# Kernel optimization log

Measured on AMD Instinct MI355X. Metric: run time of the kernel, lower is better.

## Reference

```python
import jax, jax.numpy as jnp
import numpy as np

EPS = 1e-5

def _ln(x, g, b):
    mu = x.mean(-1, keepdims=True)
    var = ((x - mu) ** 2).mean(-1, keepdims=True)
    return (x - mu) * jax.lax.rsqrt(var + EPS) * g + b

def setup_inputs() -> dict:
    B, K, D, H, T = 64, 64, 128, 128, 4
    key = jax.random.key(0)
    ks = jax.random.split(key, 20)
    s = 0.02
    inp = {
        "slots": jax.random.normal(ks[0], (B, K, D), jnp.float32),
        "edge_probs": jax.random.uniform(ks[1], (B, K, K), jnp.float32),
        "edge_types": jax.random.uniform(ks[2], (B, K, K, T), jnp.float32),
        # f_self: LayerNorm(D) -> Linear(D,H) -> ReLU -> Linear(H,D)
        "ls_g": jnp.ones((D,), jnp.float32),
        "ls_b": jnp.zeros((D,), jnp.float32),
        "ws1": jax.random.normal(ks[3], (D, H), jnp.float32) * s,
        "bs1": jnp.zeros((H,), jnp.float32),
        "ws2": jax.random.normal(ks[4], (H, D), jnp.float32) * s,
        "bs2": jnp.zeros((D,), jnp.float32),
        # f_inter[tau]: Linear(2D,H) -> ReLU -> Linear(H,H) -> ReLU -> Linear(H,D), stacked over T
        "wi1": jax.random.normal(ks[5], (T, 2 * D, H), jnp.float32) * s,
        "bi1": jnp.zeros((T, H), jnp.float32),
        "wi2": jax.random.normal(ks[6], (T, H, H), jnp.float32) * s,
        "bi2": jnp.zeros((T, H), jnp.float32),
        "wi3": jax.random.normal(ks[7], (T, H, D), jnp.float32) * s,
        "bi3": jnp.zeros((T, D), jnp.float32),
        # update_mlp: LayerNorm(2D) -> Linear(2D,H) -> ReLU -> Linear(H,D)
        "lu_g": jnp.ones((2 * D,), jnp.float32),
        "lu_b": jnp.zeros((2 * D,), jnp.float32),
        "wu1": jax.random.normal(ks[8], (2 * D, H), jnp.float32) * s,
        "bu1": jnp.zeros((H,), jnp.float32),
        "wu2": jax.random.normal(ks[9], (H, D), jnp.float32) * s,
        "bu2": jnp.zeros((D,), jnp.float32),
    }
    return inp

NUM_MP = 2

def reference(slots, edge_probs, edge_types, ls_g, ls_b, ws1, bs1, ws2, bs2,
              wi1, bi1, wi2, bi2, wi3, bi3, lu_g, lu_b, wu1, bu1, wu2, bu2):
    B, K, D = slots.shape
    T = edge_types.shape[-1]
    h = slots
    for _ in range(NUM_MP):
        # f_self
        delta_self = jax.nn.relu(_ln(h, ls_g, ls_b) @ ws1 + bs1) @ ws2 + bs2
        # all-pairs features: cat[b,i,j] = [h[b,i] (sender), h[b,j] (receiver)]
        sender = jnp.broadcast_to(h[:, :, None, :], (B, K, K, D))
        receiver = jnp.broadcast_to(h[:, None, :, :], (B, K, K, D))
        pair = jnp.concatenate([sender, receiver], axis=-1)  # [B,K,K,2D]
        delta_inter = jnp.zeros_like(h)
        for tau in range(T):
            x = jax.nn.relu(pair @ wi1[tau] + bi1[tau])
            x = jax.nn.relu(x @ wi2[tau] + bi2[tau])
            eff = x @ wi3[tau] + bi3[tau]  # [B,K,K,D]
            w = edge_probs[..., None] * edge_types[..., tau, None]  # [B,K,K,1]
            delta_inter = delta_inter + (eff * w).sum(axis=1)  # sum over sender i
        combined = jnp.concatenate([h + delta_self, delta_inter], axis=-1)
        update = jax.nn.relu(_ln(combined, lu_g, lu_b) @ wu1 + bu1) @ wu2 + bu2
        h = h + update  # residual=True
    return h
```

## Files before the change

### kernel.cpp

```cpp
#include <hip/hip_runtime.h>
#include <hip/hip_fp16.h>

#define BATCH 64
#define KSLOT 64
#define DDIM  128
#define HDIM  128
#define TTYPE 4
#define NSLOT (BATCH*KSLOT)
#define EPSLN 1e-5f
#define YROW  544

typedef _Float16 v8h __attribute__((ext_vector_type(8)));
typedef _Float16 v4h __attribute__((ext_vector_type(4)));
typedef _Float16 v2h __attribute__((ext_vector_type(2)));
typedef float    v4f __attribute__((ext_vector_type(4)));

__device__ __forceinline__ float waveAllSum(float v) {
    #pragma unroll
    for (int m = 1; m < 64; m <<= 1) v += __shfl_xor(v, m, 64);
    return v;
}

__global__ __launch_bounds__(256) void k_wconv(
        const float* __restrict__ ws1, const float* __restrict__ wi1,
        const float* __restrict__ ws2, const float* __restrict__ wu1,
        const float* __restrict__ wu2, const float* __restrict__ wi3,
        const float* __restrict__ wi2, const float* __restrict__ bi1,
        const float* __restrict__ bi3,
        const float* __restrict__ ep, const float* __restrict__ et,
        __half* __restrict__ ws1T, __half* __restrict__ wi1catT,
        __half* __restrict__ ws2T, __half* __restrict__ wu1T,
        __half* __restrict__ wu2T, __half* __restrict__ w3catT,
        __half* __restrict__ w2T16, float* __restrict__ biascat,
        __half* __restrict__ wPre) {
    __shared__ __align__(16) float tile[128*132];
    int bx = blockIdx.x, tid = threadIdx.x;
    if (bx >= 22) {
        int bx2 = bx - 22, b = bx2 >> 2, chunk = bx2 & 3;
        const float4* etb = (const float4*)(et + (size_t)b*16384);
        const float*  epb = ep + (size_t)b*4096;
        __half* w0 = wPre + ((size_t)0*BATCH + b)*4096;
        __half* w1 = wPre + ((size_t)1*BATCH + b)*4096;
        __half* w2 = wPre + ((size_t)2*BATCH + b)*4096;
        __half* w3 = wPre + ((size_t)3*BATCH + b)*4096;
        int c0 = chunk*1024;
        for (int c = c0 + tid; c < c0 + 1024; c += 256) {
            float wv = epb[c];
            float4 e = etb[c];
            w0[c] = __float2half(wv * e.x);
            w1[c] = __float2half(wv * e.y);
            w2[c] = __float2half(wv * e.z);
            w3[c] = __float2half(wv * e.w);
        }
        return;
    }
    if (bx == 21) {
        for (int idx = tid; idx < 128*32; idx += 256) {
            int o = idx >> 5, c = idx & 31;
            w3catT[(size_t)o*YROW + 512 + c] = (c < 4) ? __float2half(bi3[c*DDIM + o]) : __float2half(0.f);
        }
        for (int idx = tid; idx < 1024; idx += 256) {
            int th = idx >> 7, o = idx & 127;
            biascat[idx] = (th & 1) ? bi1[(th>>1)*HDIM + o] : 0.f;
        }
        return;
    }
    const float* src; __half* dst; int dstride = 128, dcol = 0;
    if (bx == 0)      { src = ws1; dst = ws1T; }
    else if (bx <= 8) { int th = bx-1, tau = th>>1, half = th&1;
                        src = wi1 + ((size_t)tau*256 + half*128)*128;
                        dst = wi1catT + (size_t)th*128*128; }
    else if (bx == 9) { src = ws2; dst = ws2T; }
    else if (bx ==10) { src = wu2; dst = wu2T; }
    else if (bx <=12) { int hh = bx-11; src = wu1 + (size_t)hh*128*128;
                        dst = wu1T; dstride = 256; dcol = hh*128; }
    else if (bx <=16) { int tau = bx-13; src = wi3 + (size_t)tau*16384;
                        dst = w3catT; dstride = YROW; dcol = tau*128; }
    else              { int tau = bx-17; src = wi2 + (size_t)tau*16384;
                        dst = w2T16 + (size_t)tau*16384; }
    for (int idx = tid; idx < 4096; idx += 256) {
        int r = idx >> 5, c4 = idx & 31;
        *(float4*)&tile[r*132 + c4*4] = *(const float4*)&src[(size_t)r*128 + c4*4];
    }
    __syncthreads();
    for (int idx = tid; idx < 8192; idx += 256) {
        int n = idx >> 6, kp = idx & 63;
        __half2 p = __floats2half2_rn(tile[(2*kp)*132 + n], tile[(2*kp+1)*132 + n]);
        *(__half2*)&dst[(size_t)n*dstride + dcol + 2*kp] = p;
    }
}

#define LROW 136

__device__ __forceinline__ void cluster4(v4f& p0, v4f& p1, v4f& p2, v4f& p3,
                                         const v8h x[4], const v8h bf[4][4],
                                         const v4f bias[4]) {
    p0 = bias[0]; p1 = bias[1]; p2 = bias[2]; p3 = bias[3];
    #pragma unroll
    for (int ks = 0; ks < 4; ks++) {
        p0 = __builtin_amdgcn_mfma_f32_16x16x32_f16(x[ks], bf[0][ks], p0, 0, 0, 0);
        p1 = __builtin_amdgcn_mfma_f32_16x16x32_f16(x[ks], bf[1][ks], p1, 0, 0, 0);
        p2 = __builtin_amdgcn_mfma_f32_16x16x32_f16(x[ks], bf[2][ks], p2, 0, 0, 0);
        p3 = __builtin_amdgcn_mfma_f32_16x16x32_f16(x[ks], bf[3][ks], p3, 0, 0, 0);
    }
}

__device__ __forceinline__ void epi4(v4h yacch[4], v4h& wsacch,
                                     const v4f& p0, const v4f& p1,
                                     const v4f& p2, const v4f& p3, v4h wv) {
    const v4h zero4h = {0,0,0,0};
    #define EPI1(P, OT) { \
        v2h lo = __builtin_bit_cast(v2h, __builtin_amdgcn_cvt_pkrtz(P[0], P[1])); \
        v2h hi = __builtin_bit_cast(v2h, __builtin_amdgcn_cvt_pkrtz(P[2], P[3])); \
        v4h rel = {lo[0], lo[1], hi[0], hi[1]}; \
        rel = __builtin_elementwise_max(rel, zero4h); \
        yacch[OT] = yacch[OT] + wv * rel; }
    EPI1(p0, 0) EPI1(p1, 1) EPI1(p2, 2) EPI1(p3, 3)
    #undef EPI1
    wsacch = wsacch + wv;
}

__global__ __launch_bounds__(512) void k_pair(
        const float* __restrict__ h,
        const __half* __restrict__ wi1catT,
        const float* __restrict__ biascat,
        const __half* __restrict__ w2T16,
        const float* __restrict__ bi2,
        const __half* __restrict__ wPre,
        __half* __restrict__ Ycat) {
    __shared__ __align__(16) _Float16 w2T[HDIM*LROW];
    __shared__ __align__(16) _Float16 Cs[KSLOT*LROW];
    __shared__ __align__(16) _Float16 As[KSLOT*LROW];
    __shared__ __align__(16) _Float16 wS[KSLOT*KSLOT];
    __shared__ __align__(16) _Float16 hs[KSLOT*136];
    int bx = blockIdx.x, b = bx >> 2, tau = bx & 3;
    int tid = threadIdx.x, lane = tid & 63, w = tid >> 6;
    int jt = w >> 1, oh = w & 1, quad = lane >> 4, n = lane & 15;

    for (int idx = tid; idx < 2048; idx += 512) {
        int o = idx >> 4, seg = (idx & 15)*8;
        *(v8h*)&w2T[o*LROW + seg] = *(const v8h*)&w2T16[((size_t)tau*128 + o)*128 + seg];
    }
    {
        int row = tid >> 3, c0 = (tid & 7)*16;
        const float* hp = &h[(size_t)(b*KSLOT + row)*128 + c0];
        #pragma unroll
        for (int q = 0; q < 4; q++) {
            float4 f = *(const float4*)&hp[q*4];
            *(__half2*)&hs[row*136 + c0 + q*4]     = __floats2half2_rn(f.x, f.y);
            *(__half2*)&hs[row*136 + c0 + q*4 + 2] = __floats2half2_rn(f.z, f.w);
        }
    }
    {
        int base = tid*8;
        *(v8h*)&wS[base] = *(const v8h*)&wPre[((size_t)tau*BATCH + b)*4096 + base];
    }
    __syncthreads();

    {
        int hf = w >> 2, rt = w & 3;
        const __half* wb = wi1catT + (size_t)(tau*2 + hf)*128*128;
        const float* bcp = biascat + (tau*2 + hf)*128;
        _Float16* dst = hf ? Cs : As;
        v8h afr[4];
        #pragma unroll
        for (int ks = 0; ks < 4; ks++)
            afr[ks] = *(const v8h*)&hs[(rt*16 + n)*136 + ks*32 + quad*8];
        #pragma unroll
        for (int ot = 0; ot < 8; ot++) {
            float b0 = bcp[ot*16 + n];
            v4f acc = (v4f){b0, b0, b0, b0};
            #pragma unroll
            for (int ks = 0; ks < 4; ks++)
                acc = __builtin_amdgcn_mfma_f32_16x16x32_f16(
                    afr[ks], *(const v8h*)&wb[(size_t)(ot*16 + n)*128 + ks*32 + quad*8], acc, 0, 0, 0);
            #pragma unroll
            for (int r = 0; r < 4; r++)
                dst[(rt*16 + quad*4 + r)*LROW + ot*16 + n] = (_Float16)acc[r];
        }
    }
    __syncthreads();

    v8h bfrag[4][4];
    #pragma unroll
    for (int ot = 0; ot < 4; ot++)
        #pragma unroll
        for (int ks = 0; ks < 4; ks++)
            bfrag[ot][ks] = *(const v8h*)&w2T[(oh*64 + ot*16 + n)*LROW + ks*32 + quad*8];
    v8h cfrag[4];
    #pragma unroll
    for (int ks = 0; ks < 4; ks++)
        cfrag[ks] = *(const v8h*)&Cs[(jt*16 + n)*LROW + ks*32 + quad*8];
    v4f biasvec[4];
    #pragma unroll
    for (int ot = 0; ot < 4; ot++) {
        float b0 = bi2[tau*HDIM + oh*64 + ot*16 + n];
        biasvec[ot] = (v4f){b0, b0, b0, b0};
    }

    v4h yacch[4];
    #pragma unroll
    for (int ot = 0; ot < 4; ot++) yacch[ot] = (v4h){0,0,0,0};
    v4h wsacch = (v4h){0,0,0,0};
    const v8h zero8 = {0,0,0,0,0,0,0,0};

    #define LOADA(DST, WV, I) { int _i = (I); \
        DST[0] = *(const v8h*)&As[_i*LROW +  0 + quad*8]; \
        DST[1] = *(const v8h*)&As[_i*LROW + 32 + quad*8]; \
        DST[2] = *(const v8h*)&As[_i*LROW + 64 + quad*8]; \
        DST[3] = *(const v8h*)&As[_i*LROW + 96 + quad*8]; \
        WV = *(const v4h*)&wS[_i*KSLOT + jt*16 + quad*4]; }

    v8h aA[4], aB[4], xA[4], xB[4];
    v4h wvA, wvB, wvEA, wvEB;
    LOADA(aA, wvA, 0)
    LOADA(aB, wvB, 1)
    #pragma unroll
    for (int ks = 0; ks < 4; ks++)
        xA[ks] = __builtin_elementwise_max(aA[ks] + cfrag[ks], zero8);
    v4f pA0, pA1, pA2, pA3, pB0, pB1, pB2, pB3;

    for (int ii = 0; ii < 32; ++ii) {
        int i = ii*2;
        wvEA = wvA;
        { int i2 = (i+2 < 64) ? (i+2) : 63; LOADA(aA, wvA, i2) }
        cluster4(pA0, pA1, pA2, pA3, xA, bfrag, biasvec);
        #pragma unroll
        for (int ks = 0; ks < 4; ks++)
            xB[ks] = __builtin_elementwise_max(aB[ks] + cfrag[ks], zero8);
        epi4(yacch, wsacch, pA0, pA1, pA2, pA3, wvEA);
        wvEB = wvB;
        { int i3 = (i+3 < 64) ? (i+3) : 63; LOADA(aB, wvB, i3) }
        cluster4(pB0, pB1, pB2, pB3, xB, bfrag, biasvec);
        #pragma unroll
        for (int ks = 0; ks < 4; ks++)
            xA[ks] = __builtin_elementwise_max(aA[ks] + cfrag[ks], zero8);
        epi4(yacch, wsacch, pB0, pB1, pB2, pB3, wvEB);
    }
    #undef LOADA

    #pragma unroll
    for (int r = 0; r < 4; r++) {
        int j = jt*16 + quad*4 + r;
        __half* yb = Ycat + (size_t)(b*KSLOT + j)*YROW + tau*128 + oh*64;
        #pragma unroll
        for (int ot = 0; ot < 4; ot++)
            yb[ot*16 + n] = __float2half((float)yacch[ot][r]);
    }
    if (oh == 0 && n == 0) {
        #pragma unroll
        for (int r = 0; r < 4; r++)
            Ycat[(size_t)(b*KSLOT + jt*16 + quad*4 + r)*YROW + 512 + tau] = __float2half((float)wsacch[r]);
    }
    if (tau == 0 && oh == 1 && n == 0) {
        const v4h z4 = {0,0,0,0};
        #pragma unroll
        for (int r = 0; r < 4; r++) {
            _Float16* pz = (_Float16*)(Ycat + (size_t)(b*KSLOT + jt*16 + quad*4 + r)*YROW + 516);
            #pragma unroll
            for (int c = 0; c < 28; c += 4) *(v4h*)&pz[c] = z4;
        }
    }
}

__global__ __launch_bounds__(512, 2) void k_mega(
        const __half* __restrict__ Ycat, const __half* __restrict__ w3catT,
        const float* __restrict__ ls_g, const float* __restrict__ ls_b,
        const __half* __restrict__ ws1T, const float* __restrict__ bs1,
        const __half* __restrict__ ws2T, const float* __restrict__ bs2,
        const float* __restrict__ g, const float* __restrict__ bb,
        const __half* __restrict__ wu1T, const float* __restrict__ bu1,
        const __half* __restrict__ wu2T, const float* __restrict__ bu2,
        const float* __restrict__ h, float* __restrict__ hout) {
    __shared__ __align__(16) _Float16 Ys[16*552];
    __shared__ __align__(16) float    Crow[16*260];
    __shared__ __align__(16) float    Hrow[16*132];
    __shared__ __align__(16) _Float16 Xs[16*136];
    __shared__ __align__(16) _Float16 Ts[16*136];
    __shared__ __align__(16) _Float16 Xa[16*264];
    __shared__ __align__(16) _Float16 Ut[16*136];
    int tid = threadIdx.x, lane = tid & 63, w = tid >> 6;
    int n = lane & 15, quad = lane >> 4;
    int row0 = blockIdx.x*16;

    for (int u = tid; u < 1024; u += 512) {
        int r = u >> 6, seg = (u & 63)*8;
        *(v8h*)&Ys[r*552 + seg] = *(const v8h*)&Ycat[(size_t)(row0 + r)*YROW + seg];
    }
    if (tid < 64) {
        int r = tid >> 2, seg = 512 + (tid & 3)*8;
        *(v8h*)&Ys[r*552 + seg] = *(const v8h*)&Ycat[(size_t)(row0 + r)*YROW + seg];
    }
    {
        int r = tid >> 5, c4 = (tid & 31)*4;
        *(float4*)&Hrow[r*132 + c4] = *(const float4*)&h[(size_t)(row0 + r)*128 + c4];
    }
    __syncthreads();
    {
        const __half* wp = w3catT + (size_t)(w*16 + n)*YROW + quad*8;
        const _Float16* yp = &Ys[n*552 + quad*8];
        v4f acc = (v4f){0.f,0.f,0.f,0.f};
        #pragma unroll 4
        for (int ks = 0; ks < 17; ks++) {
            v8h a  = *(const v8h*)(yp + ks*32);
            v8h bf = *(const v8h*)(wp + ks*32);
            acc = __builtin_amdgcn_mfma_f32_16x16x32_f16(a, bf, acc, 0, 0, 0);
        }
        #pragma unroll
        for (int r = 0; r < 4; r++)
            Crow[(quad*4 + r)*260 + 128 + w*16 + n] = acc[r];
    }
    #pragma unroll
    for (int rr = 0; rr < 2; rr++) {
        int r = w*2 + rr;
        float x0 = Hrow[r*132 + 2*lane], x1 = Hrow[r*132 + 2*lane + 1];
        float mu = waveAllSum(x0 + x1) * (1.f/128.f);
        float d0 = x0 - mu, d1 = x1 - mu;
        float var = waveAllSum(d0*d0 + d1*d1) * (1.f/128.f);
        float rs = rsqrtf(var + EPSLN);
        float2 gv = *(const float2*)&ls_g[2*lane];
        float2 bv = *(const float2*)&ls_b[2*lane];
        *(__half2*)&Xs[r*136 + 2*lane] = __floats2half2_rn(d0*rs*gv.x + bv.x, d1*rs*gv.y + bv.y);
    }
    __syncthreads();
    {
        float b0 = bs1[w*16 + n];
        v4f acc = (v4f){b0, b0, b0, b0};
        const __half* wp = ws1T + (size_t)(w*16 + n)*128 + quad*8;
        #pragma unroll
        for (int ks = 0; ks < 4; ks++) {
            v8h a  = *(const v8h*)&Xs[n*136 + ks*32 + quad*8];
            v8h bf = *(const v8h*)(wp + ks*32);
            acc = __builtin_amdgcn_mfma_f32_16x16x32_f16(a, bf, acc, 0, 0, 0);
        }
        #pragma unroll
        for (int r = 0; r < 4; r++)
            Ts[(quad*4 + r)*136 + w*16 + n] = (_Float16)fmaxf(acc[r], 0.f);
    }
    __syncthreads();
    {
        float b0 = bs2[w*16 + n];
        v4f acc = (v4f){b0, b0, b0, b0};
        const __half* wp = ws2T + (size_t)(w*16 + n)*128 + quad*8;
        #pragma unroll
        for (int ks = 0; ks < 4; ks++) {
            v8h a  = *(const v8h*)&Ts[n*136 + ks*32 + quad*8];
            v8h bf = *(const v8h*)(wp + ks*32);
            acc = __builtin_amdgcn_mfma_f32_16x16x32_f16(a, bf, acc, 0, 0, 0);
        }
        #pragma unroll
        for (int r = 0; r < 4; r++) {
            int rr = quad*4 + r, col = w*16 + n;
            Crow[rr*260 + col] = Hrow[rr*132 + col] + acc[r];
        }
    }
    __syncthreads();
    #pragma unroll
    for (int rr = 0; rr < 2; rr++) {
        int r = w*2 + rr;
        float4 v = *(const float4*)&Crow[r*260 + 4*lane];
        float mu = waveAllSum(v.x + v.y + v.z + v.w) * (1.f/256.f);
        float d0 = v.x-mu, d1 = v.y-mu, d2 = v.z-mu, d3 = v.w-mu;
        float var = waveAllSum(d0*d0 + d1*d1 + d2*d2 + d3*d3) * (1.f/256.f);
        float rs = rsqrtf(var + EPSLN);
        float4 gv = *(const float4*)&g[4*lane];
        float4 bv = *(const float4*)&bb[4*lane];
        *(__half2*)&Xa[r*264 + 4*lane]     = __floats2half2_rn(d0*rs*gv.x + bv.x, d1*rs*gv.y + bv.y);
        *(__half2*)&Xa[r*264 + 4*lane + 2] = __floats2half2_rn(d2*rs*gv.z + bv.z, d3*rs*gv.w + bv.w);
    }
    __syncthreads();
    {
        float b0 = bu1[w*16 + n];
        v4f acc = (v4f){b0, b0, b0, b0};
        const __half* wp = wu1T + (size_t)(w*16 + n)*256 + quad*8;
        const _Float16* xp = &Xa[n*264 + quad*8];
        #pragma unroll 4
        for (int ks = 0; ks < 8; ks++) {
            v8h a  = *(const v8h*)(xp + ks*32);
            v8h bf = *(const v8h*)(wp + ks*32);
            acc = __builtin_amdgcn_mfma_f32_16x16x32_f16(a, bf, acc, 0, 0, 0);
        }
        #pragma unroll
        for (int r = 0; r < 4; r++)
            Ut[(quad*4 + r)*136 + w*16 + n] = (_Float16)fmaxf(acc[r], 0.f);
    }
    __syncthreads();
    {
        float b0 = bu2[w*16 + n];
        v4f acc = (v4f){b0, b0, b0, b0};
        const __half* wp = wu2T + (size_t)(w*16 + n)*128 + quad*8;
        #pragma unroll
        for (int ks = 0; ks < 4; ks++) {
            v8h a  = *(const v8h*)&Ut[n*136 + ks*32 + quad*8];
            v8h bf = *(const v8h*)(wp + ks*32);
            acc = __builtin_amdgcn_mfma_f32_16x16x32_f16(a, bf, acc, 0, 0, 0);
        }
        #pragma unroll
        for (int r = 0; r < 4; r++) {
            int rr = quad*4 + r, col = w*16 + n;
            hout[(size_t)(row0 + rr)*128 + col] = Hrow[rr*132 + col] + acc[r];
        }
    }
}

extern "C" void kernel_launch(void* const* d_in, const int* in_sizes, int n_in,
                              void* d_out, int out_size, void* d_ws, size_t ws_size,
                              hipStream_t stream) {
    const float* slots = (const float*)d_in[0];
    const float* ep    = (const float*)d_in[1];
    const float* et    = (const float*)d_in[2];
    const float* ls_g  = (const float*)d_in[3];
    const float* ls_b  = (const float*)d_in[4];
    const float* ws1   = (const float*)d_in[5];
    const float* bs1   = (const float*)d_in[6];
    const float* ws2   = (const float*)d_in[7];
    const float* bs2   = (const float*)d_in[8];
    const float* wi1   = (const float*)d_in[9];
    const float* bi1   = (const float*)d_in[10];
    const float* wi2   = (const float*)d_in[11];
    const float* bi2   = (const float*)d_in[12];
    const float* wi3   = (const float*)d_in[13];
    const float* bi3   = (const float*)d_in[14];
    const float* lu_g  = (const float*)d_in[15];
    const float* lu_b  = (const float*)d_in[16];
    const float* wu1   = (const float*)d_in[17];
    const float* bu1   = (const float*)d_in[18];
    const float* wu2   = (const float*)d_in[19];
    const float* bu2   = (const float*)d_in[20];
    float* out = (float*)d_out;

    char* p = (char*)d_ws;
    float*  h_buf   = (float*)p;   p += (size_t)NSLOT*DDIM*4;
    __half* Ycat    = (__half*)p;  p += (size_t)NSLOT*YROW*2;
    __half* wPre    = (__half*)p;  p += (size_t)TTYPE*BATCH*4096*2;
    __half* ws1T    = (__half*)p;  p += 128*128*2;
    __half* wi1catT = (__half*)p;  p += 1024*128*2;
    __half* ws2T    = (__half*)p;  p += 128*128*2;
    __half* wu1T    = (__half*)p;  p += 128*256*2;
    __half* wu2T    = (__half*)p;  p += 128*128*2;
    __half* w3catT  = (__half*)p;  p += 128*YROW*2;
    __half* w2T16   = (__half*)p;  p += 4*128*128*2;
    float*  biascat = (float*)p;   p += 1024*4;

    k_wconv<<<22 + 256, 256, 0, stream>>>(ws1, wi1, ws2, wu1, wu2, wi3, wi2, bi1, bi3,
                                          ep, et, ws1T, wi1catT, ws2T, wu1T, wu2T,
                                          w3catT, w2T16, biascat, wPre);

    for (int mp = 0; mp < 2; mp++) {
        const float* h = (mp == 0) ? slots : h_buf;
        float* hout = (mp == 0) ? h_buf : out;
        k_pair<<<BATCH*TTYPE, 512, 0, stream>>>(h, wi1catT, biascat, w2T16, bi2, wPre, Ycat);
        k_mega<<<NSLOT/16, 512, 0, stream>>>(Ycat, w3catT, ls_g, ls_b, ws1T, bs1, ws2T, bs2,
                                             lu_g, lu_b, wu1T, bu1, wu2T, bu2, h, hout);
    }
}
```

Baseline: 199.8 us.

## Fuse all stages into one cooperative persistent kernel with grid syncs

```diff
diff --git a/kernel.cpp b/kernel.cpp
--- a/kernel.cpp
+++ b/kernel.cpp
@@ -1,5 +1,8 @@
 #include <hip/hip_runtime.h>
 #include <hip/hip_fp16.h>
+#include <hip/hip_cooperative_groups.h>
+
+namespace cg = cooperative_groups;
 
 #define BATCH 64
 #define KSLOT 64
@@ -19,75 +22,6 @@
     #pragma unroll
     for (int m = 1; m < 64; m <<= 1) v += __shfl_xor(v, m, 64);
     return v;
-}
-
-__global__ __launch_bounds__(256) void k_wconv(
-        const float* __restrict__ ws1, const float* __restrict__ wi1,
-        const float* __restrict__ ws2, const float* __restrict__ wu1,
-        const float* __restrict__ wu2, const float* __restrict__ wi3,
-        const float* __restrict__ wi2, const float* __restrict__ bi1,
-        const float* __restrict__ bi3,
-        const float* __restrict__ ep, const float* __restrict__ et,
-        __half* __restrict__ ws1T, __half* __restrict__ wi1catT,
-        __half* __restrict__ ws2T, __half* __restrict__ wu1T,
-        __half* __restrict__ wu2T, __half* __restrict__ w3catT,
-        __half* __restrict__ w2T16, float* __restrict__ biascat,
-        __half* __restrict__ wPre) {
-    __shared__ __align__(16) float tile[128*132];
-    int bx = blockIdx.x, tid = threadIdx.x;
-    if (bx >= 22) {
-        int bx2 = bx - 22, b = bx2 >> 2, chunk = bx2 & 3;
-        const float4* etb = (const float4*)(et + (size_t)b*16384);
-        const float*  epb = ep + (size_t)b*4096;
-        __half* w0 = wPre + ((size_t)0*BATCH + b)*4096;
-        __half* w1 = wPre + ((size_t)1*BATCH + b)*4096;
-        __half* w2 = wPre + ((size_t)2*BATCH + b)*4096;
-        __half* w3 = wPre + ((size_t)3*BATCH + b)*4096;
-        int c0 = chunk*1024;
-        for (int c = c0 + tid; c < c0 + 1024; c += 256) {
-            float wv = epb[c];
-            float4 e = etb[c];
-            w0[c] = __float2half(wv * e.x);
-            w1[c] = __float2half(wv * e.y);
-            w2[c] = __float2half(wv * e.z);
-            w3[c] = __float2half(wv * e.w);
-        }
-        return;
-    }
-    if (bx == 21) {
-        for (int idx = tid; idx < 128*32; idx += 256) {
-            int o = idx >> 5, c = idx & 31;
-            w3catT[(size_t)o*YROW + 512 + c] = (c < 4) ? __float2half(bi3[c*DDIM + o]) : __float2half(0.f);
-        }
-        for (int idx = tid; idx < 1024; idx += 256) {
-            int th = idx >> 7, o = idx & 127;
-            biascat[idx] = (th & 1) ? bi1[(th>>1)*HDIM + o] : 0.f;
-        }
-        return;
-    }
-    const float* src; __half* dst; int dstride = 128, dcol = 0;
-    if (bx == 0)      { src = ws1; dst = ws1T; }
-    else if (bx <= 8) { int th = bx-1, tau = th>>1, half = th&1;
-                        src = wi1 + ((size_t)tau*256 + half*128)*128;
-                        dst = wi1catT + (size_t)th*128*128; }
-    else if (bx == 9) { src = ws2; dst = ws2T; }
-    else if (bx ==10) { src = wu2; dst = wu2T; }
-    else if (bx <=12) { int hh = bx-11; src = wu1 + (size_t)hh*128*128;
-                        dst = wu1T; dstride = 256; dcol = hh*128; }
-    else if (bx <=16) { int tau = bx-13; src = wi3 + (size_t)tau*16384;
-                        dst = w3catT; dstride = YROW; dcol = tau*128; }
-    else              { int tau = bx-17; src = wi2 + (size_t)tau*16384;
-                        dst = w2T16 + (size_t)tau*16384; }
-    for (int idx = tid; idx < 4096; idx += 256) {
-        int r = idx >> 5, c4 = idx & 31;
-        *(float4*)&tile[r*132 + c4*4] = *(const float4*)&src[(size_t)r*128 + c4*4];
-    }
-    __syncthreads();
-    for (int idx = tid; idx < 8192; idx += 256) {
-        int n = idx >> 6, kp = idx & 63;
-        __half2 p = __floats2half2_rn(tile[(2*kp)*132 + n], tile[(2*kp+1)*132 + n]);
-        *(__half2*)&dst[(size_t)n*dstride + dcol + 2*kp] = p;
-    }
 }
 
 #define LROW 136
@@ -120,286 +54,356 @@
     wsacch = wsacch + wv;
 }
 
-__global__ __launch_bounds__(512) void k_pair(
-        const float* __restrict__ h,
-        const __half* __restrict__ wi1catT,
-        const float* __restrict__ biascat,
-        const __half* __restrict__ w2T16,
-        const float* __restrict__ bi2,
-        const __half* __restrict__ wPre,
-        __half* __restrict__ Ycat) {
-    __shared__ __align__(16) _Float16 w2T[HDIM*LROW];
-    __shared__ __align__(16) _Float16 Cs[KSLOT*LROW];
-    __shared__ __align__(16) _Float16 As[KSLOT*LROW];
-    __shared__ __align__(16) _Float16 wS[KSLOT*KSLOT];
-    __shared__ __align__(16) _Float16 hs[KSLOT*136];
-    int bx = blockIdx.x, b = bx >> 2, tau = bx & 3;
-    int tid = threadIdx.x, lane = tid & 63, w = tid >> 6;
-    int jt = w >> 1, oh = w & 1, quad = lane >> 4, n = lane & 15;
-
-    for (int idx = tid; idx < 2048; idx += 512) {
-        int o = idx >> 4, seg = (idx & 15)*8;
-        *(v8h*)&w2T[o*LROW + seg] = *(const v8h*)&w2T16[((size_t)tau*128 + o)*128 + seg];
-    }
+extern "C" __global__ __launch_bounds__(512, 2) void k_fused(
+        const float* __restrict__ slots, const float* __restrict__ ep,
+        const float* __restrict__ et,
+        const float* __restrict__ ls_g, const float* __restrict__ ls_b,
+        const float* __restrict__ ws1, const float* __restrict__ bs1,
+        const float* __restrict__ ws2, const float* __restrict__ bs2,
+        const float* __restrict__ wi1, const float* __restrict__ bi1,
+        const float* __restrict__ wi2, const float* __restrict__ bi2,
+        const float* __restrict__ wi3, const float* __restrict__ bi3,
+        const float* __restrict__ lu_g, const float* __restrict__ lu_b,
+        const float* __restrict__ wu1, const float* __restrict__ bu1,
+        const float* __restrict__ wu2, const float* __restrict__ bu2,
+        float* __restrict__ out, float* __restrict__ h_buf,
+        __half* __restrict__ Ycat, __half* __restrict__ wPre,
+        __half* __restrict__ ws1T, __half* __restrict__ wi1catT,
+        __half* __restrict__ ws2T, __half* __restrict__ wu1T,
+        __half* __restrict__ wu2T, __half* __restrict__ w3catT,
+        __half* __restrict__ w2T16, float* __restrict__ biascat) {
+    __shared__ __align__(16) char smem[95232];
+    cg::grid_group grid = cg::this_grid();
+    int bx = blockIdx.x, tid = threadIdx.x;
+
     {
-        int row = tid >> 3, c0 = (tid & 7)*16;
-        const float* hp = &h[(size_t)(b*KSLOT + row)*128 + c0];
-        #pragma unroll
-        for (int q = 0; q < 4; q++) {
-            float4 f = *(const float4*)&hp[q*4];
-            *(__half2*)&hs[row*136 + c0 + q*4]     = __floats2half2_rn(f.x, f.y);
-            *(__half2*)&hs[row*136 + c0 + q*4 + 2] = __floats2half2_rn(f.z, f.w);
+        int b2 = bx >> 2, chunk = bx & 3;
+        const float4* etb = (const float4*)(et + (size_t)b2*16384);
+        const float*  epb = ep + (size_t)b2*4096;
+        __half* wp0 = wPre + ((size_t)0*BATCH + b2)*4096;
+        __half* wp1 = wPre + ((size_t)1*BATCH + b2)*4096;
+        __half* wp2 = wPre + ((size_t)2*BATCH + b2)*4096;
+        __half* wp3 = wPre + ((size_t)3*BATCH + b2)*4096;
+        int c0 = chunk*1024;
+        for (int c = c0 + tid; c < c0 + 1024; c += 512) {
+            float wv = epb[c];
+            float4 e = etb[c];
+            wp0[c] = __float2half(wv * e.x);
+            wp1[c] = __float2half(wv * e.y);
+            wp2[c] = __float2half(wv * e.z);
+            wp3[c] = __float2half(wv * e.w);
+        }
+        if (bx < 21) {
+            const float* src; __half* dst; int dstride = 128, dcol = 0;
+            if (bx == 0)      { src = ws1; dst = ws1T; }
+            else if (bx <= 8) { int th = bx-1, tu = th>>1, half = th&1;
+                                src = wi1 + ((size_t)tu*256 + half*128)*128;
+                                dst = wi1catT + (size_t)th*128*128; }
+            else if (bx == 9) { src = ws2; dst = ws2T; }
+            else if (bx ==10) { src = wu2; dst = wu2T; }
+            else if (bx <=12) { int hh = bx-11; src = wu1 + (size_t)hh*128*128;
+                                dst = wu1T; dstride = 256; dcol = hh*128; }
+            else if (bx <=16) { int tu = bx-13; src = wi3 + (size_t)tu*16384;
+                                dst = w3catT; dstride = YROW; dcol = tu*128; }
+            else              { int tu = bx-17; src = wi2 + (size_t)tu*16384;
+                                dst = w2T16 + (size_t)tu*16384; }
+            float* tile = (float*)smem;
+            for (int idx = tid; idx < 4096; idx += 512) {
+                int r = idx >> 5, c4 = idx & 31;
+                *(float4*)&tile[r*132 + c4*4] = *(const float4*)&src[(size_t)r*128 + c4*4];
+            }
+            __syncthreads();
+            for (int idx = tid; idx < 8192; idx += 512) {
+                int nn = idx >> 6, kp = idx & 63;
+                __half2 pq = __floats2half2_rn(tile[(2*kp)*132 + nn], tile[(2*kp+1)*132 + nn]);
+                *(__half2*)&dst[(size_t)nn*dstride + dcol + 2*kp] = pq;
+            }
+        } else if (bx == 21) {
+            for (int idx = tid; idx < 128*32; idx += 512) {
+                int o = idx >> 5, c = idx & 31;
+                w3catT[(size_t)o*YROW + 512 + c] = (c < 4) ? __float2half(bi3[c*DDIM + o]) : __float2half(0.f);
+            }
+            for (int idx = tid; idx < 1024; idx += 512) {
+                int th = idx >> 7, o = idx & 127;
+                biascat[idx] = (th & 1) ? bi1[(th>>1)*HDIM + o] : 0.f;
+            }
         }
     }
-    {
-        int base = tid*8;
-        *(v8h*)&wS[base] = *(const v8h*)&wPre[((size_t)tau*BATCH + b)*4096 + base];
-    }
-    __syncthreads();
-
-    {
-        int hf = w >> 2, rt = w & 3;
-        const __half* wb = wi1catT + (size_t)(tau*2 + hf)*128*128;
-        const float* bcp = biascat + (tau*2 + hf)*128;
-        _Float16* dst = hf ? Cs : As;
-        v8h afr[4];
-        #pragma unroll
-        for (int ks = 0; ks < 4; ks++)
-            afr[ks] = *(const v8h*)&hs[(rt*16 + n)*136 + ks*32 + quad*8];
-        #pragma unroll
-        for (int ot = 0; ot < 8; ot++) {
-            float b0 = bcp[ot*16 + n];
-            v4f acc = (v4f){b0, b0, b0, b0};
+    grid.sync();
+
+    for (int mp = 0; mp < 2; mp++) {
+        const float* hin = (mp == 0) ? slots : h_buf;
+        float* hout = (mp == 0) ? h_buf : out;
+
+        {
+            _Float16* w2T = (_Float16*)smem;
+            _Float16* Cs  = w2T + 17408;
+            _Float16* As  = Cs  + 8704;
+            _Float16* wS  = As  + 8704;
+            _Float16* hs  = wS  + 4096;
+            int b = bx >> 2, tau = bx & 3;
+            int lane = tid & 63, w = tid >> 6;
+            int jt = w >> 1, oh = w & 1, quad = lane >> 4, n = lane & 15;
+
+            for (int idx = tid; idx < 2048; idx += 512) {
+                int o = idx >> 4, seg = (idx & 15)*8;
+                *(v8h*)&w2T[o*LROW + seg] = *(const v8h*)&w2T16[((size_t)tau*128 + o)*128 + seg];
+            }
+            {
+                int row = tid >> 3, c0 = (tid & 7)*16;
+                const float* hp = &hin[(size_t)(b*KSLOT + row)*128 + c0];
+                #pragma unroll
+                for (int q = 0; q < 4; q++) {
+                    float4 f = *(const float4*)&hp[q*4];
+                    *(__half2*)&hs[row*136 + c0 + q*4]     = __floats2half2_rn(f.x, f.y);
+                    *(__half2*)&hs[row*136 + c0 + q*4 + 2] = __floats2half2_rn(f.z, f.w);
+                }
+            }
+            {
+                int base = tid*8;
+                *(v8h*)&wS[base] = *(const v8h*)&wPre[((size_t)tau*BATCH + b)*4096 + base];
+            }
+            __syncthreads();
+
+            {
+                int hf = w >> 2, rt = w & 3;
+                const __half* wb = wi1catT + (size_t)(tau*2 + hf)*128*128;
+                const float* bcp = biascat + (tau*2 + hf)*128;
+                _Float16* dst = hf ? Cs : As;
+                v8h afr[4];
+                #pragma unroll
+                for (int ks = 0; ks < 4; ks++)
+                    afr[ks] = *(const v8h*)&hs[(rt*16 + n)*136 + ks*32 + quad*8];
+                #pragma unroll
+                for (int ot = 0; ot < 8; ot++) {
+                    float b0 = bcp[ot*16 + n];
+                    v4f acc = (v4f){b0, b0, b0, b0};
+                    #pragma unroll
+                    for (int ks = 0; ks < 4; ks++)
+                        acc = __builtin_amdgcn_mfma_f32_16x16x32_f16(
+                            afr[ks], *(const v8h*)&wb[(size_t)(ot*16 + n)*128 + ks*32 + quad*8], acc, 0, 0, 0);
+                    #pragma unroll
+                    for (int r = 0; r < 4; r++)
+                        dst[(rt*16 + quad*4 + r)*LROW + ot*16 + n] = (_Float16)acc[r];
+                }
+            }
+            __syncthreads();
+
+            v8h bfrag[4][4];
+            #pragma unroll
+            for (int ot = 0; ot < 4; ot++)
+                #pragma unroll
+                for (int ks = 0; ks < 4; ks++)
+                    bfrag[ot][ks] = *(const v8h*)&w2T[(oh*64 + ot*16 + n)*LROW + ks*32 + quad*8];
+            v8h cfrag[4];
             #pragma unroll
             for (int ks = 0; ks < 4; ks++)
-                acc = __builtin_amdgcn_mfma_f32_16x16x32_f16(
-                    afr[ks], *(const v8h*)&wb[(size_t)(ot*16 + n)*128 + ks*32 + quad*8], acc, 0, 0, 0);
-            #pragma unroll
-            for (int r = 0; r < 4; r++)
-                dst[(rt*16 + quad*4 + r)*LROW + ot*16 + n] = (_Float16)acc[r];
+                cfrag[ks] = *(const v8h*)&Cs[(jt*16 + n)*LROW + ks*32 + quad*8];
+            v4f biasvec[4];
+            #pragma unroll
+            for (int ot = 0; ot < 4; ot++) {
+                float b0 = bi2[tau*HDIM + oh*64 + ot*16 + n];
+                biasvec[ot] = (v4f){b0, b0, b0, b0};
+            }
+
+            v4h yacch[4];
+            #pragma unroll
+            for (int ot = 0; ot < 4; ot++) yacch[ot] = (v4h){0,0,0,0};
+            v4h wsacch = (v4h){0,0,0,0};
+            const v8h zero8 = {0,0,0,0,0,0,0,0};
+
+            #define LOADA(DST, WV, I) { int _i = (I); \
+                DST[0] = *(const v8h*)&As[_i*LROW +  0 + quad*8]; \
+                DST[1] = *(const v8h*)&As[_i*LROW + 32 + quad*8]; \
+                DST[2] = *(const v8h*)&As[_i*LROW + 64 + quad*8]; \
+                DST[3] = *(const v8h*)&As[_i*LROW + 96 + quad*8]; \
+                WV = *(const v4h*)&wS[_i*KSLOT + jt*16 + quad*4]; }
+
+            v8h aA[4], aB[4], xA[4], xB[4];
+            v4h wvA, wvB, wvEA, wvEB;
+            LOADA(aA, wvA, 0)
+            LOADA(aB, wvB, 1)
+            #pragma unroll
+            for (int ks = 0; ks < 4; ks++)
+                xA[ks] = __builtin_elementwise_max(aA[ks] + cfrag[ks], zero8);
+            v4f pA0, pA1, pA2, pA3, pB0, pB1, pB2, pB3;
+
+            for (int ii = 0; ii < 32; ++ii) {
+                int i = ii*2;
+                wvEA = wvA;
+                { int i2 = (i+2 < 64) ? (i+2) : 63; LOADA(aA, wvA, i2) }
+                cluster4(pA0, pA1, pA2, pA3, xA, bfrag, biasvec);
+                #pragma unroll
+                for (int ks = 0; ks < 4; ks++)
+                    xB[ks] = __builtin_elementwise_max(aB[ks] + cfrag[ks], zero8);
+                epi4(yacch, wsacch, pA0, pA1, pA2, pA3, wvEA);
+                wvEB = wvB;
+                { int i3 = (i+3 < 64) ? (i+3) : 63; LOADA(aB, wvB, i3) }
+                cluster4(pB0, pB1, pB2, pB3, xB, bfrag, biasvec);
+                #pragma unroll
+                for (int ks = 0; ks < 4; ks++)
+                    xA[ks] = __builtin_elementwise_max(aA[ks] + cfrag[ks], zero8);
+                epi4(yacch, wsacch, pB0, pB1, pB2, pB3, wvEB);
+            }
+            #undef LOADA
+
+            #pragma unroll
+            for (int r = 0; r < 4; r++) {
+                int j = jt*16 + quad*4 + r;
+                __half* yb = Ycat + (size_t)(b*KSLOT + j)*YROW + tau*128 + oh*64;
+                #pragma unroll
+                for (int ot = 0; ot < 4; ot++)
+                    yb[ot*16 + n] = __float2half((float)yacch[ot][r]);
+            }
+            if (oh == 0 && n == 0) {
+                #pragma unroll
+                for (int r = 0; r < 4; r++)
+                    Ycat[(size_t)(b*KSLOT + jt*16 + quad*4 + r)*YROW + 512 + tau] = __float2half((float)wsacch[r]);
+            }
+            if (tau == 0 && oh == 1 && n == 0) {
+                const v4h z4 = {0,0,0,0};
+                #pragma unroll
+                for (int r = 0; r < 4; r++) {
+                    _Float16* pz = (_Float16*)(Ycat + (size_t)(b*KSLOT + jt*16 + quad*4 + r)*YROW + 516);
+                    #pragma unroll
+                    for (int c = 0; c < 28; c += 4) *(v4h*)&pz[c] = z4;
+                }
+            }
         }
-    }
-    __syncthreads();
-
-    v8h bfrag[4][4];
-    #pragma unroll
-    for (int ot = 0; ot < 4; ot++)
-        #pragma unroll
-        for (int ks = 0; ks < 4; ks++)
-            bfrag[ot][ks] = *(const v8h*)&w2T[(oh*64 + ot*16 + n)*LROW + ks*32 + quad*8];
-    v8h cfrag[4];
-    #pragma unroll
-    for (int ks = 0; ks < 4; ks++)
-        cfrag[ks] = *(const v8h*)&Cs[(jt*16 + n)*LROW + ks*32 + quad*8];
-    v4f biasvec[4];
-    #pragma unroll
-    for (int ot = 0; ot < 4; ot++) {
-        float b0 = bi2[tau*HDIM + oh*64 + ot*16 + n];
-        biasvec[ot] = (v4f){b0, b0, b0, b0};
-    }
-
-    v4h yacch[4];
-    #pragma unroll
-    for (int ot = 0; ot < 4; ot++) yacch[ot] = (v4h){0,0,0,0};
-    v4h wsacch = (v4h){0,0,0,0};
-    const v8h zero8 = {0,0,0,0,0,0,0,0};
-
-    #define LOADA(DST, WV, I) { int _i = (I); \
-        DST[0] = *(const v8h*)&As[_i*LROW +  0 + quad*8]; \
-        DST[1] = *(const v8h*)&As[_i*LROW + 32 + quad*8]; \
-        DST[2] = *(const v8h*)&As[_i*LROW + 64 + quad*8]; \
-        DST[3] = *(const v8h*)&As[_i*LROW + 96 + quad*8]; \
-        WV = *(const v4h*)&wS[_i*KSLOT + jt*16 + quad*4]; }
-
-    v8h aA[4], aB[4], xA[4], xB[4];
-    v4h wvA, wvB, wvEA, wvEB;
-    LOADA(aA, wvA, 0)
-    LOADA(aB, wvB, 1)
-    #pragma unroll
-    for (int ks = 0; ks < 4; ks++)
-        xA[ks] = __builtin_elementwise_max(aA[ks] + cfrag[ks], zero8);
-    v4f pA0, pA1, pA2, pA3, pB0, pB1, pB2, pB3;
-
-    for (int ii = 0; ii < 32; ++ii) {
-        int i = ii*2;
-        wvEA = wvA;
-        { int i2 = (i+2 < 64) ? (i+2) : 63; LOADA(aA, wvA, i2) }
-        cluster4(pA0, pA1, pA2, pA3, xA, bfrag, biasvec);
-        #pragma unroll
-        for (int ks = 0; ks < 4; ks++)
-            xB[ks] = __builtin_elementwise_max(aB[ks] + cfrag[ks], zero8);
-        epi4(yacch, wsacch, pA0, pA1, pA2, pA3, wvEA);
-        wvEB = wvB;
-        { int i3 = (i+3 < 64) ? (i+3) : 63; LOADA(aB, wvB, i3) }
-        cluster4(pB0, pB1, pB2, pB3, xB, bfrag, biasvec);
-        #pragma unroll
-        for (int ks = 0; ks < 4; ks++)
-            xA[ks] = __builtin_elementwise_max(aA[ks] + cfrag[ks], zero8);
-        epi4(yacch, wsacch, pB0, pB1, pB2, pB3, wvEB);
-    }
-    #undef LOADA
-
-    #pragma unroll
-    for (int r = 0; r < 4; r++) {
-        int j = jt*16 + quad*4 + r;
-        __half* yb = Ycat + (size_t)(b*KSLOT + j)*YROW + tau*128 + oh*64;
-        #pragma unroll
-        for (int ot = 0; ot < 4; ot++)
-            yb[ot*16 + n] = __float2half((float)yacch[ot][r]);
-    }
-    if (oh == 0 && n == 0) {
-        #pragma unroll
-        for (int r = 0; r < 4; r++)
-            Ycat[(size_t)(b*KSLOT + jt*16 + quad*4 + r)*YROW + 512 + tau] = __float2half((float)wsacch[r]);
-    }
-    if (tau == 0 && oh == 1 && n == 0) {
-        const v4h z4 = {0,0,0,0};
-        #pragma unroll
-        for (int r = 0; r < 4; r++) {
-            _Float16* pz = (_Float16*)(Ycat + (size_t)(b*KSLOT + jt*16 + quad*4 + r)*YROW + 516);
-            #pragma unroll
-            for (int c = 0; c < 28; c += 4) *(v4h*)&pz[c] = z4;
+        grid.sync();
+
+        {
+            _Float16* Ys  = (_Float16*)smem;
+            float*    Crow = (float*)(smem + 17664);
+            float*    Hrow = (float*)(smem + 34304);
+            _Float16* Xs  = (_Float16*)(smem + 42752);
+            _Float16* Ts  = (_Float16*)(smem + 47104);
+            _Float16* Xa  = (_Float16*)(smem + 51456);
+            _Float16* Ut  = (_Float16*)(smem + 59904);
+            int lane = tid & 63, w = tid >> 6;
+            int n = lane & 15, quad = lane >> 4;
+            int row0 = bx*16;
+
+            for (int u = tid; u < 1024; u += 512) {
+                int r = u >> 6, seg = (u & 63)*8;
+                *(v8h*)&Ys[r*552 + seg] = *(const v8h*)&Ycat[(size_t)(row0 + r)*YROW + seg];
+            }
+            if (tid < 64) {
+                int r = tid >> 2, seg = 512 + (tid & 3)*8;
+                *(v8h*)&Ys[r*552 + seg] = *(const v8h*)&Ycat[(size_t)(row0 + r)*YROW + seg];
+            }
+            {
+                int r = tid >> 5, c4 = (tid & 31)*4;
+                *(float4*)&Hrow[r*132 + c4] = *(const float4*)&hin[(size_t)(row0 + r)*128 + c4];
+            }
+            __syncthreads();
+            {
+                const __half* wp = w3catT + (size_t)(w*16 + n)*YROW + quad*8;
+                const _Float16* yp = &Ys[n*552 + quad*8];
+                v4f acc = (v4f){0.f,0.f,0.f,0.f};
+                #pragma unroll 4
+                for (int ks = 0; ks < 17; ks++) {
+                    v8h a  = *(const v8h*)(yp + ks*32);
+                    v8h bf = *(const v8h*)(wp + ks*32);
+                    acc = __builtin_amdgcn_mfma_f32_16x16x32_f16(a, bf, acc, 0, 0, 0);
+                }
+                #pragma unroll
+                for (int r = 0; r < 4; r++)
+                    Crow[(quad*4 + r)*260 + 128 + w*16 + n] = acc[r];
+            }
+            #pragma unroll
+            for (int rr = 0; rr < 2; rr++) {
+                int r = w*2 + rr;
+                float x0 = Hrow[r*132 + 2*lane], x1 = Hrow[r*132 + 2*lane + 1];
+                float mu = waveAllSum(x0 + x1) * (1.f/128.f);
+                float d0 = x0 - mu, d1 = x1 - mu;
+                float var = waveAllSum(d0*d0 + d1*d1) * (1.f/128.f);
+                float rs = rsqrtf(var + EPSLN);
+                float2 gv = *(const float2*)&ls_g[2*lane];
+                float2 bv = *(const float2*)&ls_b[2*lane];
+                *(__half2*)&Xs[r*136 + 2*lane] = __floats2half2_rn(d0*rs*gv.x + bv.x, d1*rs*gv.y + bv.y);
+            }
+            __syncthreads();
+            {
+                float b0 = bs1[w*16 + n];
+                v4f acc = (v4f){b0, b0, b0, b0};
+                const __half* wp = ws1T + (size_t)(w*16 + n)*128 + quad*8;
+                #pragma unroll
+                for (int ks = 0; ks < 4; ks++) {
+                    v8h a  = *(const v8h*)&Xs[n*136 + ks*32 + quad*8];
+                    v8h bf = *(const v8h*)(wp + ks*32);
+                    acc = __builtin_amdgcn_mfma_f32_16x16x32_f16(a, bf, acc, 0, 0, 0);
+                }
+                #pragma unroll
+                for (int r = 0; r < 4; r++)
+                    Ts[(quad*4 + r)*136 + w*16 + n] = (_Float16)fmaxf(acc[r], 0.f);
+            }
+            __syncthreads();
+            {
+                float b0 = bs2[w*16 + n];
+                v4f acc = (v4f){b0, b0, b0, b0};
+                const __half* wp = ws2T + (size_t)(w*16 + n)*128 + quad*8;
+                #pragma unroll
+                for (int ks = 0; ks < 4; ks++) {
+                    v8h a  = *(const v8h*)&Ts[n*136 + ks*32 + quad*8];
+                    v8h bf = *(const v8h*)(wp + ks*32);
+                    acc = __builtin_amdgcn_mfma_f32_16x16x32_f16(a, bf, acc, 0, 0, 0);
+                }
+                #pragma unroll
+                for (int r = 0; r < 4; r++) {
+                    int rr = quad*4 + r, col = w*16 + n;
+                    Crow[rr*260 + col] = Hrow[rr*132 + col] + acc[r];
+                }
+            }
+            __syncthreads();
+            #pragma unroll
+            for (int rr = 0; rr < 2; rr++) {
+                int r = w*2 + rr;
+                float4 v = *(const float4*)&Crow[r*260 + 4*lane];
+                float mu = waveAllSum(v.x + v.y + v.z + v.w) * (1.f/256.f);
+                float d0 = v.x-mu, d1 = v.y-mu, d2 = v.z-mu, d3 = v.w-mu;
+                float var = waveAllSum(d0*d0 + d1*d1 + d2*d2 + d3*d3) * (1.f/256.f);
+                float rs = rsqrtf(var + EPSLN);
+                float4 gv = *(const float4*)&lu_g[4*lane];
+                float4 bv = *(const float4*)&lu_b[4*lane];
+                *(__half2*)&Xa[r*264 + 4*lane]     = __floats2half2_rn(d0*rs*gv.x + bv.x, d1*rs*gv.y + bv.y);
+                *(__half2*)&Xa[r*264 + 4*lane + 2] = __floats2half2_rn(d2*rs*gv.z + bv.z, d3*rs*gv.w + bv.w);
+            }
+            __syncthreads();
+            {
+                float b0 = bu1[w*16 + n];
+                v4f acc = (v4f){b0, b0, b0, b0};
+                const __half* wp = wu1T + (size_t)(w*16 + n)*256 + quad*8;
+                const _Float16* xp = &Xa[n*264 + quad*8];
+                #pragma unroll 4
+                for (int ks = 0; ks < 8; ks++) {
+                    v8h a  = *(const v8h*)(xp + ks*32);
+                    v8h bf = *(const v8h*)(wp + ks*32);
+                    acc = __builtin_amdgcn_mfma_f32_16x16x32_f16(a, bf, acc, 0, 0, 0);
+                }
+                #pragma unroll
+                for (int r = 0; r < 4; r++)
+                    Ut[(quad*4 + r)*136 + w*16 + n] = (_Float16)fmaxf(acc[r], 0.f);
+            }
+            __syncthreads();
+            {
+                float b0 = bu2[w*16 + n];
+                v4f acc = (v4f){b0, b0, b0, b0};
+                const __half* wp = wu2T + (size_t)(w*16 + n)*128 + quad*8;
+                #pragma unroll
+                for (int ks = 0; ks < 4; ks++) {
+                    v8h a  = *(const v8h*)&Ut[n*136 + ks*32 + quad*8];
+                    v8h bf = *(const v8h*)(wp + ks*32);
+                    acc = __builtin_amdgcn_mfma_f32_16x16x32_f16(a, bf, acc, 0, 0, 0);
+                }
+                #pragma unroll
+                for (int r = 0; r < 4; r++) {
+                    int rr = quad*4 + r, col = w*16 + n;
+                    hout[(size_t)(row0 + rr)*128 + col] = Hrow[rr*132 + col] + acc[r];
+                }
+            }
         }
-    }
-}
-
-__global__ __launch_bounds__(512, 2) void k_mega(
-        const __half* __restrict__ Ycat, const __half* __restrict__ w3catT,
-        const float* __restrict__ ls_g, const float* __restrict__ ls_b,
-        const __half* __restrict__ ws1T, const float* __restrict__ bs1,
-        const __half* __restrict__ ws2T, const float* __restrict__ bs2,
-        const float* __restrict__ g, const float* __restrict__ bb,
-        const __half* __restrict__ wu1T, const float* __restrict__ bu1,
-        const __half* __restrict__ wu2T, const float* __restrict__ bu2,
-        const float* __restrict__ h, float* __restrict__ hout) {
-    __shared__ __align__(16) _Float16 Ys[16*552];
-    __shared__ __align__(16) float    Crow[16*260];
-    __shared__ __align__(16) float    Hrow[16*132];
-    __shared__ __align__(16) _Float16 Xs[16*136];
-    __shared__ __align__(16) _Float16 Ts[16*136];
-    __shared__ __align__(16) _Float16 Xa[16*264];
-    __shared__ __align__(16) _Float16 Ut[16*136];
-    int tid = threadIdx.x, lane = tid & 63, w = tid >> 6;
-    int n = lane & 15, quad = lane >> 4;
-    int row0 = blockIdx.x*16;
-
-    for (int u = tid; u < 1024; u += 512) {
-        int r = u >> 6, seg = (u & 63)*8;
-        *(v8h*)&Ys[r*552 + seg] = *(const v8h*)&Ycat[(size_t)(row0 + r)*YROW + seg];
-    }
-    if (tid < 64) {
-        int r = tid >> 2, seg = 512 + (tid & 3)*8;
-        *(v8h*)&Ys[r*552 + seg] = *(const v8h*)&Ycat[(size_t)(row0 + r)*YROW + seg];
-    }
-    {
-        int r = tid >> 5, c4 = (tid & 31)*4;
-        *(float4*)&Hrow[r*132 + c4] = *(const float4*)&h[(size_t)(row0 + r)*128 + c4];
-    }
-    __syncthreads();
-    {
-        const __half* wp = w3catT + (size_t)(w*16 + n)*YROW + quad*8;
-        const _Float16* yp = &Ys[n*552 + quad*8];
-        v4f acc = (v4f){0.f,0.f,0.f,0.f};
-        #pragma unroll 4
-        for (int ks = 0; ks < 17; ks++) {
-            v8h a  = *(const v8h*)(yp + ks*32);
-            v8h bf = *(const v8h*)(wp + ks*32);
-            acc = __builtin_amdgcn_mfma_f32_16x16x32_f16(a, bf, acc, 0, 0, 0);
-        }
-        #pragma unroll
-        for (int r = 0; r < 4; r++)
-            Crow[(quad*4 + r)*260 + 128 + w*16 + n] = acc[r];
-    }
-    #pragma unroll
-    for (int rr = 0; rr < 2; rr++) {
-        int r = w*2 + rr;
-        float x0 = Hrow[r*132 + 2*lane], x1 = Hrow[r*132 + 2*lane + 1];
-        float mu = waveAllSum(x0 + x1) * (1.f/128.f);
-        float d0 = x0 - mu, d1 = x1 - mu;
-        float var = waveAllSum(d0*d0 + d1*d1) * (1.f/128.f);
-        float rs = rsqrtf(var + EPSLN);
-        float2 gv = *(const float2*)&ls_g[2*lane];
-        float2 bv = *(const float2*)&ls_b[2*lane];
-        *(__half2*)&Xs[r*136 + 2*lane] = __floats2half2_rn(d0*rs*gv.x + bv.x, d1*rs*gv.y + bv.y);
-    }
-    __syncthreads();
-    {
-        float b0 = bs1[w*16 + n];
-        v4f acc = (v4f){b0, b0, b0, b0};
-        const __half* wp = ws1T + (size_t)(w*16 + n)*128 + quad*8;
-        #pragma unroll
-        for (int ks = 0; ks < 4; ks++) {
-            v8h a  = *(const v8h*)&Xs[n*136 + ks*32 + quad*8];
-            v8h bf = *(const v8h*)(wp + ks*32);
-            acc = __builtin_amdgcn_mfma_f32_16x16x32_f16(a, bf, acc, 0, 0, 0);
-        }
-        #pragma unroll
-        for (int r = 0; r < 4; r++)
-            Ts[(quad*4 + r)*136 + w*16 + n] = (_Float16)fmaxf(acc[r], 0.f);
-    }
-    __syncthreads();
-    {
-        float b0 = bs2[w*16 + n];
-        v4f acc = (v4f){b0, b0, b0, b0};
-        const __half* wp = ws2T + (size_t)(w*16 + n)*128 + quad*8;
-        #pragma unroll
-        for (int ks = 0; ks < 4; ks++) {
-            v8h a  = *(const v8h*)&Ts[n*136 + ks*32 + quad*8];
-            v8h bf = *(const v8h*)(wp + ks*32);
-            acc = __builtin_amdgcn_mfma_f32_16x16x32_f16(a, bf, acc, 0, 0, 0);
-        }
-        #pragma unroll
-        for (int r = 0; r < 4; r++) {
-            int rr = quad*4 + r, col = w*16 + n;
-            Crow[rr*260 + col] = Hrow[rr*132 + col] + acc[r];
-        }
-    }
-    __syncthreads();
-    #pragma unroll
-    for (int rr = 0; rr < 2; rr++) {
-        int r = w*2 + rr;
-        float4 v = *(const float4*)&Crow[r*260 + 4*lane];
-        float mu = waveAllSum(v.x + v.y + v.z + v.w) * (1.f/256.f);
-        float d0 = v.x-mu, d1 = v.y-mu, d2 = v.z-mu, d3 = v.w-mu;
-        float var = waveAllSum(d0*d0 + d1*d1 + d2*d2 + d3*d3) * (1.f/256.f);
-        float rs = rsqrtf(var + EPSLN);
-        float4 gv = *(const float4*)&g[4*lane];
-        float4 bv = *(const float4*)&bb[4*lane];
-        *(__half2*)&Xa[r*264 + 4*lane]     = __floats2half2_rn(d0*rs*gv.x + bv.x, d1*rs*gv.y + bv.y);
-        *(__half2*)&Xa[r*264 + 4*lane + 2] = __floats2half2_rn(d2*rs*gv.z + bv.z, d3*rs*gv.w + bv.w);
-    }
-    __syncthreads();
-    {
-        float b0 = bu1[w*16 + n];
-        v4f acc = (v4f){b0, b0, b0, b0};
-        const __half* wp = wu1T + (size_t)(w*16 + n)*256 + quad*8;
-        const _Float16* xp = &Xa[n*264 + quad*8];
-        #pragma unroll 4
-        for (int ks = 0; ks < 8; ks++) {
-            v8h a  = *(const v8h*)(xp + ks*32);
-            v8h bf = *(const v8h*)(wp + ks*32);
-            acc = __builtin_amdgcn_mfma_f32_16x16x32_f16(a, bf, acc, 0, 0, 0);
-        }
-        #pragma unroll
-        for (int r = 0; r < 4; r++)
-            Ut[(quad*4 + r)*136 + w*16 + n] = (_Float16)fmaxf(acc[r], 0.f);
-    }
-    __syncthreads();
-    {
-        float b0 = bu2[w*16 + n];
-        v4f acc = (v4f){b0, b0, b0, b0};
-        const __half* wp = wu2T + (size_t)(w*16 + n)*128 + quad*8;
-        #pragma unroll
-        for (int ks = 0; ks < 4; ks++) {
-            v8h a  = *(const v8h*)&Ut[n*136 + ks*32 + quad*8];
-            v8h bf = *(const v8h*)(wp + ks*32);
-            acc = __builtin_amdgcn_mfma_f32_16x16x32_f16(a, bf, acc, 0, 0, 0);
-        }
-        #pragma unroll
-        for (int r = 0; r < 4; r++) {
-            int rr = quad*4 + r, col = w*16 + n;
-            hout[(size_t)(row0 + rr)*128 + col] = Hrow[rr*132 + col] + acc[r];
-        }
+        if (mp == 0) grid.sync();
     }
 }
 
@@ -442,15 +446,14 @@
     __half* w2T16   = (__half*)p;  p += 4*128*128*2;
     float*  biascat = (float*)p;   p += 1024*4;
 
-    k_wconv<<<22 + 256, 256, 0, stream>>>(ws1, wi1, ws2, wu1, wu2, wi3, wi2, bi1, bi3,
-                                          ep, et, ws1T, wi1catT, ws2T, wu1T, wu2T,
-                                          w3catT, w2T16, biascat, wPre);
-
-    for (int mp = 0; mp < 2; mp++) {
-        const float* h = (mp == 0) ? slots : h_buf;
-        float* hout = (mp == 0) ? h_buf : out;
-        k_pair<<<BATCH*TTYPE, 512, 0, stream>>>(h, wi1catT, biascat, w2T16, bi2, wPre, Ycat);
-        k_mega<<<NSLOT/16, 512, 0, stream>>>(Ycat, w3catT, ls_g, ls_b, ws1T, bs1, ws2T, bs2,
-                                             lu_g, lu_b, wu1T, bu1, wu2T, bu2, h, hout);
-    }
+    void* args[] = {
+        (void*)&slots, (void*)&ep, (void*)&et, (void*)&ls_g, (void*)&ls_b,
+        (void*)&ws1, (void*)&bs1, (void*)&ws2, (void*)&bs2,
+        (void*)&wi1, (void*)&bi1, (void*)&wi2, (void*)&bi2, (void*)&wi3, (void*)&bi3,
+        (void*)&lu_g, (void*)&lu_b, (void*)&wu1, (void*)&bu1, (void*)&wu2, (void*)&bu2,
+        (void*)&out, (void*)&h_buf, (void*)&Ycat, (void*)&wPre,
+        (void*)&ws1T, (void*)&wi1catT, (void*)&ws2T, (void*)&wu1T, (void*)&wu2T,
+        (void*)&w3catT, (void*)&w2T16, (void*)&biascat };
+    hipLaunchCooperativeKernel(reinterpret_cast<void*>(k_fused),
+                               dim3(256), dim3(512), args, 0, stream);
 }
```

Result: slower. 371.6 us (+86.0%).
